# Kernel optimization log

Hardware: AMD Instinct MI355X
Metric: run time of the kernel (lower is better)

The kernel has to match this reference:

```python
import jax, jax.numpy as jnp
import numpy as np

C = 512

def _conv1x1(x, w, b):
    # x: [B, C, T], w: [O, C], b: [O] -> [B, O, T]
    return jnp.einsum('oc,bct->bot', w, x) + b[None, :, None]

def setup_inputs() -> dict:
    key = jax.random.key(0)
    ks = jax.random.split(key, 9)
    B, T = 8, 2048
    s = 1.0 / np.sqrt(C)
    inp = {'x': jax.random.normal(ks[0], (B, C, T), dtype=jnp.float32)}
    names = ['theta', 'phi', 'g', 'w']
    for i, n in enumerate(names):
        inp[f'w_{n}'] = jax.random.uniform(ks[1 + 2 * i], (C, C), jnp.float32, -s, s)
        inp[f'b_{n}'] = jax.random.uniform(ks[2 + 2 * i], (C,), jnp.float32, -s, s)
    return inp

def reference(x, w_theta, b_theta, w_phi, b_phi, w_g, b_g, w_w, b_w):
    relu = jax.nn.relu
    feat_theta = relu(_conv1x1(x, w_theta, b_theta))          # [B, C, T]
    feat_phi = relu(_conv1x1(x, w_phi, b_phi))                # [B, C, T]
    # scores: Q^T K over channel dim -> [B, T, T]
    scores = jnp.einsum('bci,bcj->bij', feat_theta, feat_phi)
    attn = jax.nn.softmax(scores, axis=2)                     # [B, T, T]
    feat_g = relu(_conv1x1(x, w_g, b_g))                      # [B, C, T]
    # attention-weighted V: [B, T, T] x [B, T, C] -> [B, T, C] -> [B, C, T]
    feature = jnp.einsum('bij,bcj->bci', attn, feat_g)
    w_feature = relu(_conv1x1(feature, w_w, b_w))
    return w_feature + x
```

## Files before the change

kernel.cpp:

```cpp
#include <hip/hip_runtime.h>
#include <math.h>

#define C_DIM 512
#define T_DIM 2048
#define B_DIM 8

typedef _Float16 f16;
typedef __attribute__((ext_vector_type(8))) _Float16 half8;
typedef __attribute__((ext_vector_type(4))) _Float16 half4;
typedef __attribute__((ext_vector_type(4))) float floatx4;

typedef __attribute__((address_space(1))) void gvoid;
typedef __attribute__((address_space(3))) void lvoid;

__device__ __forceinline__ void gl_lds16(const f16* g, f16* l) {
    __builtin_amdgcn_global_load_lds((gvoid*)g, (lvoid*)l, 16, 0, 0);
}

__global__ __launch_bounds__(256) void convert_w_kernel(
    const float* __restrict__ w0, const float* __restrict__ w1,
    const float* __restrict__ w2, const float* __restrict__ w3,
    f16* __restrict__ o0, f16* __restrict__ o1,
    f16* __restrict__ o2, f16* __restrict__ o3)
{
    const float* src; f16* dst;
    switch (blockIdx.z) {
        case 0:  src = w0; dst = o0; break;
        case 1:  src = w1; dst = o1; break;
        case 2:  src = w2; dst = o2; break;
        default: src = w3; dst = o3; break;
    }
    const int idx = (blockIdx.x * 256 + threadIdx.x) * 4;
    const float4 v = *(const float4*)(src + idx);
    half4 h; h[0] = (f16)v.x; h[1] = (f16)v.y; h[2] = (f16)v.z; h[3] = (f16)v.w;
    *(half4*)(dst + idx) = h;
}

__global__ __launch_bounds__(256) void concat_bias_kernel(
    const float* __restrict__ b0, const float* __restrict__ b1,
    float* __restrict__ o)
{
    const int i = blockIdx.x * 256 + threadIdx.x;
    o[i] = (i < 512) ? b0[i] : b1[i - 512];
}

__global__ __launch_bounds__(256) void transpose_x_kernel(
    const float* __restrict__ x, f16* __restrict__ xt)
{
    __shared__ float xs[32][33];
    const int b  = blockIdx.z;
    const int t0 = blockIdx.x * 32, c0 = blockIdx.y * 32;
    const float* xb = x + (size_t)b * C_DIM * T_DIM;
    const int r = threadIdx.x >> 3, q = threadIdx.x & 7;

    const float4 v = *(const float4*)(xb + (size_t)(c0 + r) * T_DIM + t0 + q * 4);
    xs[r][q * 4 + 0] = v.x; xs[r][q * 4 + 1] = v.y;
    xs[r][q * 4 + 2] = v.z; xs[r][q * 4 + 3] = v.w;
    __syncthreads();

    f16* xtb = xt + (size_t)b * C_DIM * T_DIM;
    half4 h;
    h[0] = (f16)xs[q * 4 + 0][r]; h[1] = (f16)xs[q * 4 + 1][r];
    h[2] = (f16)xs[q * 4 + 2][r]; h[3] = (f16)xs[q * 4 + 3][r];
    *(half4*)(xtb + (size_t)(t0 + r) * C_DIM + c0 + q * 4) = h;
}

template<int MODE>
__global__ __launch_bounds__(256) void gemm_tn(
    const f16* __restrict__ A, size_t sA, int lda,
    const f16* __restrict__ B, size_t sB, int ldb,
    void* __restrict__ Cp, size_t sC, int ldc,
    const float* __restrict__ bias,
    const float* __restrict__ resid, size_t sR,
    int K)
{
    __shared__ __align__(16) f16 As[2][128 * 32];
    __shared__ __align__(16) f16 Bs[2][128 * 32];

    const int gx = gridDim.x;
    const int flat = blockIdx.y * gx + blockIdx.x;
    const int jsc = gx >> 2;
    const int sh = (jsc <= 1) ? 0 : (31 - __builtin_clz(jsc));
    const int s = flat >> 4, rem = flat & 15;
    const int i0 = ((s >> sh) * 4 + (rem >> 2)) * 128;
    const int j0 = (((jsc <= 1) ? 0 : (s & (jsc - 1))) * 4 + (rem & 3)) * 128;

    const int bz = blockIdx.z;
    A += (size_t)bz * sA;
    B += (size_t)bz * sB;

    const int tid  = threadIdx.x;
    const int lane = tid & 63;
    const int wave = tid >> 6;
    const int wy = wave >> 1, wx = wave & 1;
    const int quad = lane >> 4, l16 = lane & 15;

    const int cb0 = wave * 128,      cb1 = wave * 128 + 64;
    const int r0  = (cb0 + lane) >> 2, r1 = (cb1 + lane) >> 2;
    const int q0  = ((cb0 + lane) & 3) ^ (r0 & 3);
    const int q1  = ((cb1 + lane) & 3) ^ (r1 & 3);

    const f16* gA0 = A + (size_t)(i0 + r0) * lda + q0 * 8;
    const f16* gA1 = A + (size_t)(i0 + r1) * lda + q1 * 8;
    const f16* gB0 = B + (size_t)(j0 + r0) * ldb + q0 * 8;
    const f16* gB1 = B + (size_t)(j0 + r1) * ldb + q1 * 8;

    const int xa = (quad ^ (l16 & 3)) << 3;

    floatx4 acc[4][4] = {};

    gl_lds16(gA0, &As[0][cb0 * 8]);
    gl_lds16(gA1, &As[0][cb1 * 8]);
    gl_lds16(gB0, &Bs[0][cb0 * 8]);
    gl_lds16(gB1, &Bs[0][cb1 * 8]);

    for (int k0 = 0; k0 < K; k0 += 32) {
        const int p = (k0 >> 5) & 1;
        __syncthreads();
        if (k0 + 32 < K) {
            const int pn = p ^ 1;
            gl_lds16(gA0 + k0 + 32, &As[pn][cb0 * 8]);
            gl_lds16(gA1 + k0 + 32, &As[pn][cb1 * 8]);
            gl_lds16(gB0 + k0 + 32, &Bs[pn][cb0 * 8]);
            gl_lds16(gB1 + k0 + 32, &Bs[pn][cb1 * 8]);
        }

        half8 af[4], bf[4];
        #pragma unroll
        for (int mi = 0; mi < 4; ++mi)
            af[mi] = *(const half8*)&As[p][(wy * 64 + mi * 16 + l16) * 32 + xa];
        #pragma unroll
        for (int ni = 0; ni < 4; ++ni)
            bf[ni] = *(const half8*)&Bs[p][(wx * 64 + ni * 16 + l16) * 32 + xa];
        #pragma unroll
        for (int mi = 0; mi < 4; ++mi)
            #pragma unroll
            for (int ni = 0; ni < 4; ++ni)
                acc[mi][ni] = __builtin_amdgcn_mfma_f32_16x16x32_f16(
                    af[mi], bf[ni], acc[mi][ni], 0, 0, 0);
    }

    #pragma unroll
    for (int mi = 0; mi < 4; ++mi) {
        #pragma unroll
        for (int ni = 0; ni < 4; ++ni) {
            const int col = j0 + wx * 64 + ni * 16 + l16;
            #pragma unroll
            for (int r = 0; r < 4; ++r) {
                const int row = i0 + wy * 64 + mi * 16 + quad * 4 + r;
                float v = acc[mi][ni][r];
                if (MODE == 1) { v += bias[col]; v = v > 0.f ? v : 0.f; }
                if (MODE == 2) { v += bias[row]; v = v > 0.f ? v : 0.f; }
                if (MODE == 3) {
                    v += bias[row];
                    v = v > 0.f ? v : 0.f;
                    v += resid[(size_t)bz * sR + (size_t)row * ldc + col];
                    ((float*)Cp)[(size_t)bz * sC + (size_t)row * ldc + col] = v;
                } else {
                    ((f16*)Cp)[(size_t)bz * sC + (size_t)row * ldc + col] = (f16)v;
                }
            }
        }
    }
}

__global__ __launch_bounds__(256) void softmax_f16_kernel(f16* __restrict__ S)
{
    f16* p = S + (size_t)blockIdx.x * T_DIM;
    const int tid = threadIdx.x;

    half8 hv = *((const half8*)p + tid);
    float v[8];
    float lmax = -1e30f;
    #pragma unroll
    for (int c = 0; c < 8; ++c) { v[c] = (float)hv[c]; lmax = fmaxf(lmax, v[c]); }
    #pragma unroll
    for (int off = 32; off; off >>= 1)
        lmax = fmaxf(lmax, __shfl_down(lmax, off));
    __shared__ float redm[4];
    if ((tid & 63) == 0) redm[tid >> 6] = lmax;
    __syncthreads();
    const float m = fmaxf(fmaxf(redm[0], redm[1]), fmaxf(redm[2], redm[3]));

    float lsum = 0.f;
    #pragma unroll
    for (int c = 0; c < 8; ++c) { v[c] = __expf(v[c] - m); lsum += v[c]; }
    #pragma unroll
    for (int off = 32; off; off >>= 1)
        lsum += __shfl_down(lsum, off);
    __shared__ float reds[4];
    if ((tid & 63) == 0) reds[tid >> 6] = lsum;
    __syncthreads();
    const float inv = 1.f / (reds[0] + reds[1] + reds[2] + reds[3]);

    #pragma unroll
    for (int c = 0; c < 8; ++c) hv[c] = (f16)(v[c] * inv);
    *((half8*)p + tid) = hv;
}

extern "C" void kernel_launch(void* const* d_in, const int* in_sizes, int n_in,
                              void* d_out, int out_size, void* d_ws, size_t ws_size,
                              hipStream_t stream)
{
    const float* x       = (const float*)d_in[0];
    const float* w_theta = (const float*)d_in[1];
    const float* b_theta = (const float*)d_in[2];
    const float* w_phi   = (const float*)d_in[3];
    const float* b_phi   = (const float*)d_in[4];
    const float* w_g     = (const float*)d_in[5];
    const float* b_g     = (const float*)d_in[6];
    const float* w_w     = (const float*)d_in[7];
    const float* b_w     = (const float*)d_in[8];
    float* out = (float*)d_out;

    const size_t FE = (size_t)B_DIM * C_DIM * T_DIM;
    const size_t TC = (size_t)T_DIM * C_DIM;
    const size_t TT = (size_t)T_DIM * T_DIM;

    f16* xt      = (f16*)d_ws;
    f16* wtp     = xt + FE;
    f16* wg_h    = wtp + 524288;
    f16* ww_h    = wg_h + 262144;
    float* btp   = (float*)(ww_h + 262144);
    f16* tp      = (f16*)(btp + 1024);
    f16* g       = tp + (size_t)B_DIM * T_DIM * 1024;
    f16* scores  = g + FE;
    f16* feature = tp;

    const dim3 blk(256);

    convert_w_kernel<<<dim3(256, 1, 4), blk, 0, stream>>>(
        w_theta, w_phi, w_g, w_w, wtp, wtp + 262144, wg_h, ww_h);
    concat_bias_kernel<<<dim3(4), blk, 0, stream>>>(b_theta, b_phi, btp);
    transpose_x_kernel<<<dim3(T_DIM / 32, C_DIM / 32, B_DIM), blk, 0, stream>>>(x, xt);

    gemm_tn<1><<<dim3(1024 / 128, T_DIM / 128, B_DIM), blk, 0, stream>>>(
        xt, TC, C_DIM, wtp, 0, C_DIM, tp, (size_t)T_DIM * 1024, 1024,
        btp, nullptr, 0, C_DIM);
    gemm_tn<2><<<dim3(T_DIM / 128, C_DIM / 128, B_DIM), blk, 0, stream>>>(
        wg_h, 0, C_DIM, xt, TC, C_DIM, g, TC, T_DIM, b_g, nullptr, 0, C_DIM);
    gemm_tn<0><<<dim3(T_DIM / 128, T_DIM / 128, B_DIM), blk, 0, stream>>>(
        tp, (size_t)T_DIM * 1024, 1024, tp + 512, (size_t)T_DIM * 1024, 1024,
        scores, TT, T_DIM, nullptr, nullptr, 0, C_DIM);
    softmax_f16_kernel<<<dim3(B_DIM * T_DIM), blk, 0, stream>>>(scores);
    gemm_tn<0><<<dim3(C_DIM / 128, T_DIM / 128, B_DIM), blk, 0, stream>>>(
        scores, TT, T_DIM, g, TC, T_DIM, feature, TC, C_DIM, nullptr, nullptr, 0, T_DIM);
    gemm_tn<3><<<dim3(T_DIM / 128, C_DIM / 128, B_DIM), blk, 0, stream>>>(
        ww_h, 0, C_DIM, feature, TC, C_DIM, out, TC, T_DIM, b_w, x, TC, C_DIM);
}
```

Measured before the change: 298.1 us.

## Replace direct global-to-LDS loads with register-staged two-deep prefetch in GEMM

The GEMM main loop now loads tiles from global memory into registers two iterations ahead, then writes them to swizzled LDS with ordinary vector stores, replacing the global_load_lds direct-to-LDS path. The goal is to hide global load latency behind more compute by prefetching further ahead. In exchange it uses more VGPRs for the staged data and issues extra LDS store instructions. It also changes the global-side swizzle, so global reads are now contiguous per row.

```diff
diff --git a/kernel.cpp b/kernel.cpp
--- a/kernel.cpp
+++ b/kernel.cpp
@@ -9,13 +9,6 @@
 typedef __attribute__((ext_vector_type(8))) _Float16 half8;
 typedef __attribute__((ext_vector_type(4))) _Float16 half4;
 typedef __attribute__((ext_vector_type(4))) float floatx4;
-
-typedef __attribute__((address_space(1))) void gvoid;
-typedef __attribute__((address_space(3))) void lvoid;
-
-__device__ __forceinline__ void gl_lds16(const f16* g, f16* l) {
-    __builtin_amdgcn_global_load_lds((gvoid*)g, (lvoid*)l, 16, 0, 0);
-}
 
 __global__ __launch_bounds__(256) void convert_w_kernel(
     const float* __restrict__ w0, const float* __restrict__ w1,
@@ -95,35 +88,42 @@
     const int wy = wave >> 1, wx = wave & 1;
     const int quad = lane >> 4, l16 = lane & 15;
 
-    const int cb0 = wave * 128,      cb1 = wave * 128 + 64;
-    const int r0  = (cb0 + lane) >> 2, r1 = (cb1 + lane) >> 2;
-    const int q0  = ((cb0 + lane) & 3) ^ (r0 & 3);
-    const int q1  = ((cb1 + lane) & 3) ^ (r1 & 3);
-
-    const f16* gA0 = A + (size_t)(i0 + r0) * lda + q0 * 8;
-    const f16* gA1 = A + (size_t)(i0 + r1) * lda + q1 * 8;
-    const f16* gB0 = B + (size_t)(j0 + r0) * ldb + q0 * 8;
-    const f16* gB1 = B + (size_t)(j0 + r1) * ldb + q1 * 8;
+    const int row1 = tid >> 2, ch = tid & 3;
+    const int row2 = row1 + 64;
+    const int w1 = row1 * 32 + ((ch ^ (row1 & 3)) << 3);
+    const int w2 = row2 * 32 + ((ch ^ (row2 & 3)) << 3);
+
+    const f16* gA1 = A + (size_t)(i0 + row1) * lda + ch * 8;
+    const f16* gA2 = A + (size_t)(i0 + row2) * lda + ch * 8;
+    const f16* gB1 = B + (size_t)(j0 + row1) * ldb + ch * 8;
+    const f16* gB2 = B + (size_t)(j0 + row2) * ldb + ch * 8;
 
     const int xa = (quad ^ (l16 & 3)) << 3;
 
+    const int nt = K >> 5;
+    float4 rA1[2], rA2[2], rB1[2], rB2[2];
+
+    rA1[0] = *(const float4*)(gA1);      rA2[0] = *(const float4*)(gA2);
+    rB1[0] = *(const float4*)(gB1);      rB2[0] = *(const float4*)(gB2);
+    rA1[1] = *(const float4*)(gA1 + 32); rA2[1] = *(const float4*)(gA2 + 32);
+    rB1[1] = *(const float4*)(gB1 + 32); rB2[1] = *(const float4*)(gB2 + 32);
+
     floatx4 acc[4][4] = {};
 
-    gl_lds16(gA0, &As[0][cb0 * 8]);
-    gl_lds16(gA1, &As[0][cb1 * 8]);
-    gl_lds16(gB0, &Bs[0][cb0 * 8]);
-    gl_lds16(gB1, &Bs[0][cb1 * 8]);
-
-    for (int k0 = 0; k0 < K; k0 += 32) {
-        const int p = (k0 >> 5) & 1;
+    for (int t = 0; t < nt; ++t) {
+        const int p = t & 1;
+        *(float4*)&As[p][w1] = rA1[p];
+        *(float4*)&As[p][w2] = rA2[p];
+        *(float4*)&Bs[p][w1] = rB1[p];
+        *(float4*)&Bs[p][w2] = rB2[p];
+        if (t + 2 < nt) {
+            const int off = (t + 2) * 32;
+            rA1[p] = *(const float4*)(gA1 + off);
+            rA2[p] = *(const float4*)(gA2 + off);
+            rB1[p] = *(const float4*)(gB1 + off);
+            rB2[p] = *(const float4*)(gB2 + off);
+        }
         __syncthreads();
-        if (k0 + 32 < K) {
-            const int pn = p ^ 1;
-            gl_lds16(gA0 + k0 + 32, &As[pn][cb0 * 8]);
-            gl_lds16(gA1 + k0 + 32, &As[pn][cb1 * 8]);
-            gl_lds16(gB0 + k0 + 32, &Bs[pn][cb0 * 8]);
-            gl_lds16(gB1 + k0 + 32, &Bs[pn][cb1 * 8]);
-        }
 
         half8 af[4], bf[4];
         #pragma unroll
```

Measured after the change: 621.3 us. 108% more time.
